# Kernel optimization log

Measured on AMD Instinct MI355X. Metric: run time of the kernel, lower is better.

Reference implementation:

```python
import jax, jax.numpy as jnp
from jax import lax
import numpy as np

N, F_IN, D_MODEL = 8192, 128, 256
D_INNER, D_STATE, D_CONV, DT_RANK = 512, 16, 4, 16  # expand=2, d_state=16, d_conv=4, dt_rank=ceil(256/16)
BN_EPS = 1e-5


def setup_inputs() -> dict:
    key = jax.random.key(0)
    ks = jax.random.split(key, 12)
    rn = lambda k, s, sc: jax.random.normal(k, s, jnp.float32) * sc
    x = rn(ks[0], (N, F_IN), 1.0)
    # normalized dense adjacency (row sums ~1)
    adj = jax.random.uniform(ks[1], (N, N), jnp.float32) * (2.0 / N)
    w_gcn = rn(ks[2], (F_IN, D_MODEL), 1.0 / np.sqrt(F_IN))
    b_gcn = rn(ks[3], (D_MODEL,), 0.02)
    bn_gamma = jnp.ones((D_MODEL,), jnp.float32)
    bn_beta = jnp.zeros((D_MODEL,), jnp.float32)
    w_in = rn(ks[4], (2 * D_INNER, D_MODEL), 1.0 / np.sqrt(D_MODEL))
    conv_w = rn(ks[5], (D_INNER, D_CONV), 1.0 / np.sqrt(D_CONV))
    conv_b = rn(ks[6], (D_INNER,), 0.02)
    w_xproj = rn(ks[7], (DT_RANK + 2 * D_STATE, D_INNER), 1.0 / np.sqrt(D_INNER))
    w_dt = rn(ks[8], (D_INNER, DT_RANK), 1.0 / np.sqrt(DT_RANK))
    b_dt = rn(ks[9], (D_INNER,), 0.1)
    A_log = jnp.log(jnp.broadcast_to(jnp.arange(1, D_STATE + 1, dtype=jnp.float32), (D_INNER, D_STATE)))
    D_skip = jnp.ones((D_INNER,), jnp.float32)
    w_out = rn(ks[10], (D_MODEL, D_INNER), 1.0 / np.sqrt(D_INNER))
    return dict(x=x, adj=adj, w_gcn=w_gcn, b_gcn=b_gcn, bn_gamma=bn_gamma, bn_beta=bn_beta,
                w_in=w_in, conv_w=conv_w, conv_b=conv_b, w_xproj=w_xproj, w_dt=w_dt,
                b_dt=b_dt, A_log=A_log, D_skip=D_skip, w_out=w_out)


def _forward(x, adj, w_gcn, b_gcn, bn_gamma, bn_beta, w_in, conv_w, conv_b,
             w_xproj, w_dt, b_dt, A_log, D_skip, w_out):
    # --- GCN layer: adj @ (x @ W) + b ---
    h = adj @ (x @ w_gcn) + b_gcn            # (N, D_MODEL)
    h = jax.nn.relu(h)
    # dropout: eval mode -> identity
    # --- BatchNorm1d (batch statistics, biased var, as torch training norm) ---
    mean = jnp.mean(h, axis=0)
    var = jnp.var(h, axis=0)
    h = (h - mean) * lax.rsqrt(var + BN_EPS) * bn_gamma + bn_beta  # (N, D_MODEL)

    # --- Mamba block, batch=1, seq_len=N ---
    xz = h @ w_in.T                          # (N, 2*D_INNER)
    xm, z = jnp.split(xz, 2, axis=-1)        # (N, D_INNER) each

    # causal depthwise conv1d (kernel D_CONV) + SiLU
    xp = jnp.pad(xm, ((D_CONV - 1, 0), (0, 0)))
    xc = conv_b + sum(xp[i:i + N] * conv_w[:, i] for i in range(D_CONV))  # (N, D_INNER)
    xc = jax.nn.silu(xc)

    # input-dependent SSM parameters
    x_dbl = xc @ w_xproj.T                   # (N, DT_RANK + 2*D_STATE)
    dt_r = x_dbl[:, :DT_RANK]
    B = x_dbl[:, DT_RANK:DT_RANK + D_STATE]  # (N, D_STATE)
    C = x_dbl[:, DT_RANK + D_STATE:]         # (N, D_STATE)
    dt = jax.nn.softplus(dt_r @ w_dt.T + b_dt)  # (N, D_INNER)

    A = -jnp.exp(A_log)                      # (D_INNER, D_STATE)
    deltaA = jnp.exp(dt[:, :, None] * A[None])                 # (N, D_INNER, D_STATE)
    deltaBu = dt[:, :, None] * B[:, None, :] * xc[:, :, None]  # (N, D_INNER, D_STATE)

    def step(hs, inp):
        dA, dBu, c = inp
        hs = dA * hs + dBu                   # (D_INNER, D_STATE)
        return hs, hs @ c                    # emit (D_INNER,)

    h0 = jnp.zeros((D_INNER, D_STATE), xc.dtype)
    _, ys = lax.scan(step, h0, (deltaA, deltaBu, C))  # ys: (N, D_INNER)

    y = ys + D_skip * xc
    y = y * jax.nn.silu(z)
    out_m = y @ w_out.T                      # (N, D_MODEL)
    return out_m + h                         # residual


def reference(x, adj, w_gcn, b_gcn, bn_gamma, bn_beta, w_in, conv_w, conv_b,
              w_xproj, w_dt, b_dt, A_log, D_skip, w_out):
    return _forward(x, adj, w_gcn, b_gcn, bn_gamma, bn_beta, w_in, conv_w, conv_b,
                    w_xproj, w_dt, b_dt, A_log, D_skip, w_out)
```

## Files before the change

kernel.cpp:

```cpp
#include <hip/hip_runtime.h>
#include <stdint.h>

#define NN   8192
#define FIN  128
#define DM   256
#define DI   512
#define DST  16
#define NC   256
#define CL   32

typedef short bf16x8 __attribute__((ext_vector_type(8)));
typedef float f32x4 __attribute__((ext_vector_type(4)));
union FragU { unsigned u[4]; uint4 u4; bf16x8 v; };

__device__ __forceinline__ unsigned short f2bf(float x){
  unsigned u = __float_as_uint(x);
  return (unsigned short)((u + 0x7FFFu + ((u >> 16) & 1u)) >> 16);
}
__device__ __forceinline__ unsigned pack2(float a, float b){
  return (unsigned)f2bf(a) | ((unsigned)f2bf(b) << 16);
}
__device__ __forceinline__ unsigned pack2rn(float a, float b){
  unsigned ua = __float_as_uint(a) + 0x8000u;
  unsigned ub = __float_as_uint(b) + 0x8000u;
  return __builtin_amdgcn_perm(ub, ua, 0x07060302u);
}
__device__ __forceinline__ uint4 packA8(float4 a, float4 b){
  uint4 w;
  w.x = pack2rn(a.x, a.y); w.y = pack2rn(a.z, a.w);
  w.z = pack2rn(b.x, b.y); w.w = pack2rn(b.z, b.w);
  return w;
}
__device__ __forceinline__ float bf2f(unsigned short u){
  return __uint_as_float(((unsigned)u) << 16);
}
__device__ __forceinline__ float sigmoidf_(float x){ return 1.f / (1.f + __expf(-x)); }
__device__ __forceinline__ f32x4 zero4(){ f32x4 z; z[0]=0.f; z[1]=0.f; z[2]=0.f; z[3]=0.f; return z; }

#define ASYNC16(g, l) __builtin_amdgcn_global_load_lds( \
    (const __attribute__((address_space(1))) void*)(g), \
    (__attribute__((address_space(3))) void*)(l), 16, 0, 0)
#define WAITLGKM0 asm volatile("s_waitcnt lgkmcnt(0)" ::: "memory")
#define BARRIER  asm volatile("s_barrier" ::: "memory")

constexpr size_t OFF_XWT   = 0;
constexpr size_t OFF_HB    = OFF_XWT   + (size_t)DM*NN*2;
constexpr size_t OFF_HBNB  = OFF_HB    + (size_t)NN*DM*2;
constexpr size_t OFF_WINB  = OFF_HBNB  + (size_t)NN*DM*2;
constexpr size_t OFF_WXPB  = OFF_WINB  + (size_t)1024*256*2;
constexpr size_t OFF_WOUTB = OFF_WXPB  + (size_t)48*512*2;
constexpr size_t OFF_XMB   = OFF_WOUTB + (size_t)256*512*2;
constexpr size_t OFF_ZB    = OFF_XMB   + (size_t)NN*DI*2;
constexpr size_t OFF_XCB   = OFF_ZB    + (size_t)NN*DI*2;
constexpr size_t OFF_XDBL  = OFF_XCB   + (size_t)NN*DI*2;
constexpr size_t OFF_DT    = OFF_XDBL  + (size_t)NN*48*4;
constexpr size_t OFF_PF    = OFF_DT    + (size_t)NN*DI*4;
constexpr size_t OFF_CY    = OFF_PF    + (size_t)NC*DI*DST*8;
constexpr size_t OFF_YB    = OFF_CY    + (size_t)NC*DI*DST*4;
constexpr size_t OFF_BNS   = OFF_YB    + (size_t)NN*DI*2;
constexpr size_t OFF_BNS2  = OFF_BNS   + 256*4;
constexpr size_t WS_NEED   = OFF_BNS2  + 256*4;
constexpr size_t OFF_HP    = OFF_PF;

__global__ __launch_bounds__(256) void prep_kernel(
    const float* __restrict__ w_in, const float* __restrict__ w_xp, const float* __restrict__ w_out,
    unsigned short* __restrict__ o_in, unsigned short* __restrict__ o_xp, unsigned short* __restrict__ o_out)
{
  int i = blockIdx.x * 256 + threadIdx.x;
  if (i < 1024*256) o_in[i]  = f2bf(w_in[i]);
  if (i < 48*512)   o_xp[i]  = f2bf(w_xp[i]);
  if (i < 256*512)  o_out[i] = f2bf(w_out[i]);
}

__global__ __launch_bounds__(256) void gemm1_kernel(
    const float* __restrict__ x, const float* __restrict__ w, unsigned short* __restrict__ xwT)
{
  __shared__ float xs[16*128];
  const int t = threadIdx.x;
  const int m0 = blockIdx.x * 16;
  {
    int r = t >> 4, c0 = (t & 15) * 8;
    const float* src = x + (size_t)(m0 + r)*FIN + c0;
    *(float4*)&xs[r*128 + c0]     = *(const float4*)src;
    *(float4*)&xs[r*128 + c0 + 4] = *(const float4*)(src + 4);
  }
  __syncthreads();
  const int n = t;
  float acc[16];
  #pragma unroll
  for (int m = 0; m < 16; ++m) acc[m] = 0.f;
  for (int k = 0; k < 128; k += 4){
    float w0 = w[(size_t)k*DM + n];
    float w1 = w[(size_t)(k+1)*DM + n];
    float w2 = w[(size_t)(k+2)*DM + n];
    float w3 = w[(size_t)(k+3)*DM + n];
    #pragma unroll
    for (int m = 0; m < 16; ++m){
      float4 xv = *(const float4*)&xs[m*128 + k];
      acc[m] = fmaf(xv.x, w0, acc[m]);
      acc[m] = fmaf(xv.y, w1, acc[m]);
      acc[m] = fmaf(xv.z, w2, acc[m]);
      acc[m] = fmaf(xv.w, w3, acc[m]);
    }
  }
  unsigned outp[8];
  #pragma unroll
  for (int m = 0; m < 8; ++m) outp[m] = pack2(acc[2*m], acc[2*m+1]);
  unsigned short* dst = xwT + (size_t)n*NN + m0;
  ((uint4*)dst)[0] = *(uint4*)&outp[0];
  ((uint4*)dst)[1] = *(uint4*)&outp[4];
}

__global__ __launch_bounds__(512, 1) void gemm2_kernel(
    const float* __restrict__ adj, const unsigned short* __restrict__ xwT,
    float* __restrict__ hp)
{
  extern __shared__ char lds[];
  const int t = threadIdx.x;
  const int wave = t >> 6, lane = t & 63, r = lane & 15, q = lane >> 4;
  const int wm = wave & 1, wn = wave >> 1;
  const int mt = (int)blockIdx.x >> 1, ks = (int)blockIdx.x & 1;
  const int m0 = mt * 64;
  const int kb = ks * 4096;

  const int arow = t >> 3, aseg = t & 7;
  const float* asrc = adj + (size_t)(m0 + arow)*NN + kb + aseg*8;
  const int awOff = (arow*32 + ((aseg + arow) & 7)*4) * 4;
  const unsigned short* bsrc[4];
  int bwOff[4];
  #pragma unroll
  for (int j = 0; j < 4; ++j){
    int si = t + 512*j;
    int bn = si >> 3, bc = si & 7;
    bsrc[j]  = xwT + (size_t)bn*NN + kb + bc*8;
    bwOff[j] = 8192 + (bn*32 + ((bc + bn) & 7)*4) * 4;
  }

  f32x4 acc[2][4];
  #pragma unroll
  for (int mi = 0; mi < 2; ++mi)
    #pragma unroll
    for (int ni = 0; ni < 4; ++ni) acc[mi][ni] = zero4();

  int aro[2][2], bro[2][4];
  #pragma unroll
  for (int ks2 = 0; ks2 < 2; ++ks2){
    int g = ks2*4 + q;
    #pragma unroll
    for (int mi = 0; mi < 2; ++mi){
      int m = wm*32 + mi*16 + r;
      aro[ks2][mi] = (m*32 + ((g + m) & 7)*4) * 4;
    }
    #pragma unroll
    for (int ni = 0; ni < 4; ++ni){
      int n = wn*64 + ni*16 + r;
      bro[ks2][ni] = 8192 + (n*32 + ((g + n) & 7)*4) * 4;
    }
  }

  float4 arA[2], arB[2];
  uint4  brr[2][4];

  arA[0] = *(const float4*)(asrc);
  arB[0] = *(const float4*)(asrc + 4);
  #pragma unroll
  for (int j = 0; j < 4; ++j) brr[0][j] = *(const uint4*)(bsrc[j]);
  arA[1] = *(const float4*)(asrc + 64);
  arB[1] = *(const float4*)(asrc + 68);
  #pragma unroll
  for (int j = 0; j < 4; ++j) brr[1][j] = *(const uint4*)(bsrc[j] + 64);
  *(uint4*)(lds + awOff) = packA8(arA[0], arB[0]);
  #pragma unroll
  for (int j = 0; j < 4; ++j) *(uint4*)(lds + bwOff[j]) = brr[0][j];
  WAITLGKM0; BARRIER;

  #pragma unroll 2
  for (int k = 0; k < 64; ++k){
    char* Lb = lds + (k & 1)*40960;
    FragU fa[2][2], fb[2][4];
    #pragma unroll
    for (int ks2 = 0; ks2 < 2; ++ks2){
      #pragma unroll
      for (int mi = 0; mi < 2; ++mi) fa[ks2][mi].u4 = *(const uint4*)(Lb + aro[ks2][mi]);
      #pragma unroll
      for (int ni = 0; ni < 4; ++ni) fb[ks2][ni].u4 = *(const uint4*)(Lb + bro[ks2][ni]);
    }
    if (k + 2 < 64){
      int off = (k + 2) * 64;
      arA[k & 1] = *(const float4*)(asrc + off);
      arB[k & 1] = *(const float4*)(asrc + off + 4);
      #pragma unroll
      for (int j = 0; j < 4; ++j) brr[k & 1][j] = *(const uint4*)(bsrc[j] + off);
    }
    if (k + 1 < 64){
      char* Lw = lds + ((k + 1) & 1)*40960;
      const int b = (k + 1) & 1;
      *(uint4*)(Lw + awOff) = packA8(arA[b], arB[b]);
      #pragma unroll
      for (int j = 0; j < 4; ++j) *(uint4*)(Lw + bwOff[j]) = brr[b][j];
    }
    #pragma unroll
    for (int ks2 = 0; ks2 < 2; ++ks2)
      #pragma unroll
      for (int mi = 0; mi < 2; ++mi)
        #pragma unroll
        for (int ni = 0; ni < 4; ++ni)
          acc[mi][ni] = __builtin_amdgcn_mfma_f32_16x16x32_bf16(fa[ks2][mi].v, fb[ks2][ni].v, acc[mi][ni], 0, 0, 0);
    WAITLGKM0; BARRIER;
  }

  float* hpo = hp + (size_t)ks * ((size_t)NN * DM);
  #pragma unroll
  for (int mi = 0; mi < 2; ++mi)
    #pragma unroll
    for (int ni = 0; ni < 4; ++ni){
      const int n = wn*64 + ni*16 + r;
      #pragma unroll
      for (int jr = 0; jr < 4; ++jr){
        const int m = m0 + wm*32 + mi*16 + q*4 + jr;
        hpo[(size_t)m*DM + n] = acc[mi][ni][jr];
      }
    }
}

__global__ __launch_bounds__(256) void hred_kernel(
    const float* __restrict__ hp, const float* __restrict__ b_gcn,
    unsigned short* __restrict__ hb, float* __restrict__ bns, float* __restrict__ bns2)
{
  const size_t NND = (size_t)NN * DM;
  const int c = threadIdx.x;
  const int m0 = blockIdx.x * 32;
  const float bias = b_gcn[c];
  float s1 = 0.f, s2 = 0.f;
  #pragma unroll 8
  for (int rr = 0; rr < 32; ++rr){
    size_t idx = (size_t)(m0 + rr)*DM + c;
    float v = hp[idx] + hp[NND + idx] + bias;
    v = fmaxf(v, 0.f);
    hb[idx] = f2bf(v);
    s1 += v; s2 += v*v;
  }
  atomicAdd(bns + c, s1);
  atomicAdd(bns2 + c, s2);
}

__global__ __launch_bounds__(256) void bnapply_kernel(
    const unsigned short* __restrict__ hb, const float* __restrict__ s1, const float* __restrict__ s2,
    const float* __restrict__ gamma, const float* __restrict__ beta,
    unsigned short* __restrict__ hbnb)
{
  int base = (blockIdx.x*256 + threadIdx.x) * 2;
  int c0 = base & (DM - 1);
  ushort2 hv = *(const ushort2*)(hb + base);
  float mA = s1[c0] * (1.f/NN),   mB = s1[c0+1] * (1.f/NN);
  float vA = s2[c0] * (1.f/NN) - mA*mA, vB = s2[c0+1] * (1.f/NN) - mB*mB;
  float iA = rsqrtf(vA + 1e-5f), iB = rsqrtf(vB + 1e-5f);
  float a = (bf2f(hv.x) - mA)*iA*gamma[c0]   + beta[c0];
  float b = (bf2f(hv.y) - mB)*iB*gamma[c0+1] + beta[c0+1];
  ushort2 o; o.x = f2bf(a); o.y = f2bf(b);
  *(ushort2*)(hbnb + base) = o;
}

__global__ __launch_bounds__(256) void gemm3_kernel(
    const unsigned short* __restrict__ Ab, const unsigned short* __restrict__ Wb,
    unsigned short* __restrict__ xmb, unsigned short* __restrict__ zb)
{
  __shared__ uint4 alds[2048];
  const int t = threadIdx.x;
  const int wave = t >> 6, lane = t & 63, r = lane & 15, q = lane >> 4;
  const int mb = ((int)blockIdx.x & 127) * 64;
  const int nb = ((int)blockIdx.x >> 7) * 128;
  const int wm = wave & 1, wn = wave >> 1;

  #pragma unroll
  for (int j = 0; j < 8; ++j){
    int si = j*256 + t;
    int row = si >> 5, dg = si & 31;
    int sg = dg ^ (row & 31);
    ASYNC16(Ab + (size_t)(mb + row)*DM + sg*8, (char*)alds + si*16);
  }
  __syncthreads();

  f32x4 acc[2][4];
  #pragma unroll
  for (int mi = 0; mi < 2; ++mi)
    #pragma unroll
    for (int ni = 0; ni < 4; ++ni) acc[mi][ni] = zero4();

  const unsigned short* bp[4];
  #pragma unroll
  for (int ni = 0; ni < 4; ++ni)
    bp[ni] = Wb + (size_t)(nb + wn*64 + ni*16 + r)*DM + q*8;
  FragU fb[4];
  #pragma unroll
  for (int ni = 0; ni < 4; ++ni) fb[ni].u4 = *(const uint4*)bp[ni];

  #pragma unroll
  for (int it = 0; it < 8; ++it){
    FragU fbn[4];
    if (it < 7){
      #pragma unroll
      for (int ni = 0; ni < 4; ++ni) fbn[ni].u4 = *(const uint4*)(bp[ni] + (it+1)*32);
    }
    FragU fa[2];
    #pragma unroll
    for (int mi = 0; mi < 2; ++mi){
      int row = wm*32 + mi*16 + r;
      int g = it*4 + q;
      fa[mi].u4 = alds[row*32 + (g ^ (row & 31))];
    }
    #pragma unroll
    for (int mi = 0; mi < 2; ++mi)
      #pragma unroll
      for (int ni = 0; ni < 4; ++ni)
        acc[mi][ni] = __builtin_amdgcn_mfma_f32_16x16x32_bf16(fa[mi].v, fb[ni].v, acc[mi][ni], 0, 0, 0);
    if (it < 7){
      #pragma unroll
      for (int ni = 0; ni < 4; ++ni) fb[ni] = fbn[ni];
    }
  }
  #pragma unroll
  for (int mi = 0; mi < 2; ++mi)
    #pragma unroll
    for (int ni = 0; ni < 4; ++ni){
      int nc = nb + wn*64 + ni*16 + r;
      unsigned short* dst = (nc < 512) ? (xmb + nc) : (zb + (nc - 512));
      #pragma unroll
      for (int jr = 0; jr < 4; ++jr){
        int m = mb + wm*32 + mi*16 + q*4 + jr;
        dst[(size_t)m*DI] = f2bf(acc[mi][ni][jr]);
      }
    }
}

__global__ __launch_bounds__(256) void conv_kernel(
    const unsigned short* __restrict__ xmb, const float* __restrict__ conv_w, const float* __restrict__ conv_b,
    unsigned short* __restrict__ xcb)
{
  const int d0 = threadIdx.x * 2;
  const int n0 = blockIdx.x * 32;
  float4 wa = *(const float4*)(conv_w + (size_t)d0*4);
  float4 wb = *(const float4*)(conv_w + (size_t)d0*4 + 4);
  float2 bias = *(const float2*)(conv_b + d0);
  float x0a=0.f,x1a=0.f,x2a=0.f, x0b=0.f,x1b=0.f,x2b=0.f;
  #pragma unroll
  for (int j = 0; j < 3; ++j){
    int n = n0 - 3 + j;
    float va = 0.f, vb = 0.f;
    if (n >= 0){
      ushort2 u = *(const ushort2*)(xmb + (size_t)n*DI + d0);
      va = bf2f(u.x); vb = bf2f(u.y);
    }
    if (j == 0){ x0a = va; x0b = vb; }
    else if (j == 1){ x1a = va; x1b = vb; }
    else { x2a = va; x2b = vb; }
  }
  for (int j = 0; j < 32; ++j){
    int n = n0 + j;
    ushort2 u = *(const ushort2*)(xmb + (size_t)n*DI + d0);
    float x3a = bf2f(u.x), x3b = bf2f(u.y);
    float sa = bias.x + wa.x*x0a + wa.y*x1a + wa.z*x2a + wa.w*x3a;
    float sb = bias.y + wb.x*x0b + wb.y*x1b + wb.z*x2b + wb.w*x3b;
    float va = sa * sigmoidf_(sa);
    float vb = sb * sigmoidf_(sb);
    ushort2 o; o.x = f2bf(va); o.y = f2bf(vb);
    *(ushort2*)(xcb + (size_t)n*DI + d0) = o;
    x0a=x1a; x1a=x2a; x2a=x3a;
    x0b=x1b; x1b=x2b; x2b=x3b;
  }
}

__global__ __launch_bounds__(256) void gemm4_kernel(
    const unsigned short* __restrict__ Ab, const unsigned short* __restrict__ Wb,
    const float* __restrict__ w_dt, const float* __restrict__ b_dt,
    float* __restrict__ xdbl, float* __restrict__ dt)
{
  __shared__ uint4 alds[2048];
  __shared__ float xr2[32*16];
  const int t = threadIdx.x;
  const int wave = t >> 6, lane = t & 63, r = lane & 15, q = lane >> 4;
  const int m0 = (int)blockIdx.x * 32;
  #pragma unroll
  for (int j = 0; j < 8; ++j){
    int si = j*256 + t;
    int row = si >> 6, dg = si & 63;
    int sg = dg ^ (row & 31);
    ASYNC16(Ab + (size_t)(m0 + row)*DI + sg*8, (char*)alds + si*16);
  }
  __syncthreads();
  f32x4 acc[2][3];
  #pragma unroll
  for (int mi = 0; mi < 2; ++mi)
    #pragma unroll
    for (int ni = 0; ni < 3; ++ni) acc[mi][ni] = zero4();
  const int kq = wave * 128;
  const unsigned short* bp[3];
  #pragma unroll
  for (int ni = 0; ni < 3; ++ni) bp[ni] = Wb + (size_t)(ni*16 + r)*DI + kq + q*8;
  FragU fb[3];
  #pragma unroll
  for (int ni = 0; ni < 3; ++ni) fb[ni].u4 = *(const uint4*)bp[ni];
  #pragma unroll
  for (int it = 0; it < 4; ++it){
    FragU fbn[3];
    if (it < 3){
      #pragma unroll
      for (int ni = 0; ni < 3; ++ni) fbn[ni].u4 = *(const uint4*)(bp[ni] + (it+1)*32);
    }
    FragU fa[2];
    #pragma unroll
    for (int mi = 0; mi < 2; ++mi){
      int row = mi*16 + r;
      int g = (kq >> 3) + it*4 + q;
      fa[mi].u4 = alds[row*64 + (g ^ (row & 31))];
    }
    #pragma unroll
    for (int mi = 0; mi < 2; ++mi)
      #pragma unroll
      for (int ni = 0; ni < 3; ++ni)
        acc[mi][ni] = __builtin_amdgcn_mfma_f32_16x16x32_bf16(fa[mi].v, fb[ni].v, acc[mi][ni], 0, 0, 0);
    if (it < 3){
      #pragma unroll
      for (int ni = 0; ni < 3; ++ni) fb[ni] = fbn[ni];
    }
  }
  __syncthreads();
  float* red = (float*)alds;
  if (wave > 0){
    int base = ((wave - 1)*64 + lane)*24;
    #pragma unroll
    for (int mi = 0; mi < 2; ++mi)
      #pragma unroll
      for (int ni = 0; ni < 3; ++ni)
        #pragma unroll
        for (int jr = 0; jr < 4; ++jr)
          red[base + (mi*3 + ni)*4 + jr] = acc[mi][ni][jr];
  }
  __syncthreads();
  if (wave == 0){
    #pragma unroll
    for (int w = 0; w < 3; ++w){
      int base = (w*64 + lane)*24;
      #pragma unroll
      for (int mi = 0; mi < 2; ++mi)
        #pragma unroll
        for (int ni = 0; ni < 3; ++ni)
          #pragma unroll
          for (int jr = 0; jr < 4; ++jr)
            acc[mi][ni][jr] += red[base + (mi*3 + ni)*4 + jr];
    }
    #pragma unroll
    for (int mi = 0; mi < 2; ++mi)
      #pragma unroll
      for (int ni = 0; ni < 3; ++ni)
        #pragma unroll
        for (int jr = 0; jr < 4; ++jr)
          xdbl[(size_t)(m0 + mi*16 + q*4 + jr)*48 + ni*16 + r] = acc[mi][ni][jr];
    #pragma unroll
    for (int mi = 0; mi < 2; ++mi)
      #pragma unroll
      for (int jr = 0; jr < 4; ++jr)
        xr2[(mi*16 + q*4 + jr)*16 + r] = acc[mi][0][jr];
  }
  __syncthreads();
  const int d0 = t * 2;
  const float4* wp0 = (const float4*)(w_dt + (size_t)d0*16);
  const float4* wp1 = (const float4*)(w_dt + (size_t)(d0+1)*16);
  float4 wA0 = wp0[0], wA1 = wp0[1], wA2 = wp0[2], wA3 = wp0[3];
  float4 wB0 = wp1[0], wB1 = wp1[1], wB2 = wp1[2], wB3 = wp1[3];
  float2 bb = *(const float2*)(b_dt + d0);
  for (int j = 0; j < 32; ++j){
    const float4* xp = (const float4*)(xr2 + j*16);
    float4 a0 = xp[0], a1 = xp[1], a2 = xp[2], a3 = xp[3];
    float sA = bb.x, sB = bb.y;
    sA += wA0.x*a0.x + wA0.y*a0.y + wA0.z*a0.z + wA0.w*a0.w;
    sA += wA1.x*a1.x + wA1.y*a1.y + wA1.z*a1.z + wA1.w*a1.w;
    sA += wA2.x*a2.x + wA2.y*a2.y + wA2.z*a2.z + wA2.w*a2.w;
    sA += wA3.x*a3.x + wA3.y*a3.y + wA3.z*a3.z + wA3.w*a3.w;
    sB += wB0.x*a0.x + wB0.y*a0.y + wB0.z*a0.z + wB0.w*a0.w;
    sB += wB1.x*a1.x + wB1.y*a1.y + wB1.z*a1.z + wB1.w*a1.w;
    sB += wB2.x*a2.x + wB2.y*a2.y + wB2.z*a2.z + wB2.w*a2.w;
    sB += wB3.x*a3.x + wB3.y*a3.y + wB3.z*a3.z + wB3.w*a3.w;
    float oA = (sA > 20.f) ? sA : log1pf(__expf(sA));
    float oB = (sB > 20.f) ? sB : log1pf(__expf(sB));
    *(float2*)(dt + (size_t)(m0 + j)*DI + d0) = make_float2(oA, oB);
  }
}

__global__ __launch_bounds__(256) void scanA_kernel(
    const float* __restrict__ dt, const unsigned short* __restrict__ xcb,
    const float* __restrict__ xdbl, const float* __restrict__ A_log,
    float2* __restrict__ PF)
{
  __shared__ float Bs[CL*DST];
  const int t = threadIdx.x;
  const int c = (int)blockIdx.x >> 1;
  const int d = (((int)blockIdx.x & 1) << 8) + t;
  #pragma unroll
  for (int j = 0; j < 2; ++j){
    int idx = t + 256*j;
    Bs[idx] = xdbl[(size_t)(c*CL + (idx >> 4))*48 + 16 + (idx & 15)];
  }
  __syncthreads();
  float Av[DST], hs[DST];
  {
    const float4* Ap = (const float4*)(A_log + (size_t)d*DST);
    #pragma unroll
    for (int s4 = 0; s4 < 4; ++s4){
      float4 a4 = Ap[s4];
      Av[s4*4+0] = -__expf(a4.x); Av[s4*4+1] = -__expf(a4.y);
      Av[s4*4+2] = -__expf(a4.z); Av[s4*4+3] = -__expf(a4.w);
    }
  }
  #pragma unroll
  for (int s = 0; s < DST; ++s) hs[s] = 0.f;
  float sdt = 0.f;
  const size_t rb = (size_t)c*CL*DI + d;
  float dtv = dt[rb], xcv = bf2f(xcb[rb]);
  for (int tt = 0; tt < CL; ++tt){
    float dtn = 0.f, xcn = 0.f;
    if (tt + 1 < CL){
      dtn = dt[rb + (size_t)(tt+1)*DI];
      xcn = bf2f(xcb[rb + (size_t)(tt+1)*DI]);
    }
    float u = dtv * xcv;
    sdt += dtv;
    float bv[DST];
    *(float4*)&bv[0]  = *(const float4*)&Bs[tt*16];
    *(float4*)&bv[4]  = *(const float4*)&Bs[tt*16 + 4];
    *(float4*)&bv[8]  = *(const float4*)&Bs[tt*16 + 8];
    *(float4*)&bv[12] = *(const float4*)&Bs[tt*16 + 12];
    #pragma unroll
    for (int s = 0; s < DST; ++s)
      hs[s] = __expf(dtv * Av[s]) * hs[s] + u * bv[s];
    dtv = dtn; xcv = xcn;
  }
  float4* out = (float4*)(PF + (size_t)c*(DI*DST) + (size_t)d*DST);
  #pragma unroll
  for (int j = 0; j < 8; ++j){
    float4 v;
    v.x = __expf(Av[2*j] * sdt);   v.y = hs[2*j];
    v.z = __expf(Av[2*j+1] * sdt); v.w = hs[2*j+1];
    out[j] = v;
  }
}

__global__ __launch_bounds__(128) void scanB_kernel(
    const float2* __restrict__ PF, float* __restrict__ Cy)
{
  const int ds = (int)blockIdx.x*128 + (int)threadIdx.x;
  float2 A0[16], A1[16];
  #pragma unroll
  for (int j = 0; j < 16; ++j) A0[j] = PF[(size_t)j*8192 + ds];
  #pragma unroll
  for (int j = 0; j < 16; ++j) A1[j] = PF[(size_t)(16 + j)*8192 + ds];
  float cy = 0.f;
  Cy[ds] = 0.f;
  #pragma unroll
  for (int g = 0; g < 16; ++g){
    #pragma unroll
    for (int j = 0; j < 16; ++j){
      int i = g*16 + j;
      if (i < NC - 1){
        float2 pf = (g & 1) ? A1[j] : A0[j];
        cy = pf.x * cy + pf.y;
        Cy[(size_t)(i + 1)*8192 + ds] = cy;
      }
    }
    int gn = g + 2;
    if (gn < 16){
      #pragma unroll
      for (int j = 0; j < 16; ++j){
        float2 v = PF[(size_t)(gn*16 + j)*8192 + ds];
        if (g & 1) A1[j] = v; else A0[j] = v;
      }
    }
  }
}

__global__ __launch_bounds__(256) void scanC_kernel(
    const float* __restrict__ dt, const unsigned short* __restrict__ xcb,
    const float* __restrict__ xdbl, const float* __restrict__ A_log,
    const float* __restrict__ Cy, const float* __restrict__ Dskip,
    const unsigned short* __restrict__ zb, unsigned short* __restrict__ yb)
{
  __shared__ float Bs[CL*DST];
  __shared__ float Cs[CL*DST];
  const int t = threadIdx.x;
  const int c = (int)blockIdx.x >> 1;
  const int d = (((int)blockIdx.x & 1) << 8) + t;
  #pragma unroll
  for (int j = 0; j < 2; ++j){
    int idx = t + 256*j;
    int tg = c*CL + (idx >> 4);
    Bs[idx] = xdbl[(size_t)tg*48 + 16 + (idx & 15)];
    Cs[idx] = xdbl[(size_t)tg*48 + 32 + (idx & 15)];
  }
  __syncthreads();
  float Av[DST], hs[DST];
  {
    const float4* Ap = (const float4*)(A_log + (size_t)d*DST);
    #pragma unroll
    for (int s4 = 0; s4 < 4; ++s4){
      float4 a4 = Ap[s4];
      Av[s4*4+0] = -__expf(a4.x); Av[s4*4+1] = -__expf(a4.y);
      Av[s4*4+2] = -__expf(a4.z); Av[s4*4+3] = -__expf(a4.w);
    }
  }
  {
    const float4* hp4 = (const float4*)(Cy + (size_t)c*(DI*DST) + (size_t)d*DST);
    #pragma unroll
    for (int s4 = 0; s4 < 4; ++s4){
      float4 h4 = hp4[s4];
      hs[s4*4+0] = h4.x; hs[s4*4+1] = h4.y; hs[s4*4+2] = h4.z; hs[s4*4+3] = h4.w;
    }
  }
  const float Dv = Dskip[d];
  const size_t rb = (size_t)c*CL*DI + d;
  float dtv = dt[rb], xcv = bf2f(xcb[rb]);
  unsigned short zv0 = zb[rb];
  for (int tt = 0; tt < CL; ++tt){
    float dtn = 0.f, xcn = 0.f;
    unsigned short zn = 0;
    if (tt + 1 < CL){
      dtn = dt[rb + (size_t)(tt+1)*DI];
      xcn = bf2f(xcb[rb + (size_t)(tt+1)*DI]);
      zn  = zb[rb + (size_t)(tt+1)*DI];
    }
    float u = dtv * xcv;
    float bv[DST], cv[DST];
    *(float4*)&bv[0]  = *(const float4*)&Bs[tt*16];
    *(float4*)&bv[4]  = *(const float4*)&Bs[tt*16 + 4];
    *(float4*)&bv[8]  = *(const float4*)&Bs[tt*16 + 8];
    *(float4*)&bv[12] = *(const float4*)&Bs[tt*16 + 12];
    *(float4*)&cv[0]  = *(const float4*)&Cs[tt*16];
    *(float4*)&cv[4]  = *(const float4*)&Cs[tt*16 + 4];
    *(float4*)&cv[8]  = *(const float4*)&Cs[tt*16 + 8];
    *(float4*)&cv[12] = *(const float4*)&Cs[tt*16 + 12];
    float y0 = 0.f, y1 = 0.f;
    #pragma unroll
    for (int s = 0; s < DST; s += 2){
      hs[s]   = __expf(dtv * Av[s])   * hs[s]   + u * bv[s];
      hs[s+1] = __expf(dtv * Av[s+1]) * hs[s+1] + u * bv[s+1];
      y0 += hs[s]   * cv[s];
      y1 += hs[s+1] * cv[s+1];
    }
    float z = bf2f(zv0);
    float yf = ((y0 + y1) + Dv * xcv) * (z * sigmoidf_(z));
    yb[rb + (size_t)tt*DI] = f2bf(yf);
    dtv = dtn; xcv = xcn; zv0 = zn;
  }
}

__global__ __launch_bounds__(512) void gemm5_kernel(
    const unsigned short* __restrict__ yb, const unsigned short* __restrict__ Wb,
    const unsigned short* __restrict__ hbnb, float* __restrict__ out)
{
  __shared__ uint4 alds[2048];
  const int t = threadIdx.x;
  const int wave = t >> 6, lane = t & 63, r = lane & 15, q = lane >> 4;
  const int m0 = (int)blockIdx.x * 32;
  #pragma unroll
  for (int j = 0; j < 4; ++j){
    int si = j*512 + t;
    int row = si >> 6, dg = si & 63;
    int sg = dg ^ (row & 31);
    ASYNC16(yb + (size_t)(m0 + row)*DI + sg*8, (char*)alds + si*16);
  }
  __syncthreads();
  f32x4 acc[2][2];
  #pragma unroll
  for (int mi = 0; mi < 2; ++mi)
    #pragma unroll
    for (int ni = 0; ni < 2; ++ni) acc[mi][ni] = zero4();
  const int nw = wave * 32;
  const unsigned short* bp0 = Wb + (size_t)(nw + r)*DI + q*8;
  const unsigned short* bp1 = Wb + (size_t)(nw + 16 + r)*DI + q*8;
  FragU fb0, fb1;
  fb0.u4 = *(const uint4*)bp0;
  fb1.u4 = *(const uint4*)bp1;
  #pragma unroll
  for (int it = 0; it < 16; ++it){
    FragU fn0, fn1;
    if (it < 15){
      fn0.u4 = *(const uint4*)(bp0 + (it+1)*32);
      fn1.u4 = *(const uint4*)(bp1 + (it+1)*32);
    }
    FragU fa[2];
    #pragma unroll
    for (int mi = 0; mi < 2; ++mi){
      int row = mi*16 + r;
      int g = it*4 + q;
      fa[mi].u4 = alds[row*64 + (g ^ (row & 31))];
    }
    acc[0][0] = __builtin_amdgcn_mfma_f32_16x16x32_bf16(fa[0].v, fb0.v, acc[0][0], 0, 0, 0);
    acc[0][1] = __builtin_amdgcn_mfma_f32_16x16x32_bf16(fa[0].v, fb1.v, acc[0][1], 0, 0, 0);
    acc[1][0] = __builtin_amdgcn_mfma_f32_16x16x32_bf16(fa[1].v, fb0.v, acc[1][0], 0, 0, 0);
    acc[1][1] = __builtin_amdgcn_mfma_f32_16x16x32_bf16(fa[1].v, fb1.v, acc[1][1], 0, 0, 0);
    if (it < 15){ fb0 = fn0; fb1 = fn1; }
  }
  #pragma unroll
  for (int mi = 0; mi < 2; ++mi)
    #pragma unroll
    for (int ni = 0; ni < 2; ++ni){
      const int n = nw + ni*16 + r;
      #pragma unroll
      for (int jr = 0; jr < 4; ++jr){
        const int m = m0 + mi*16 + q*4 + jr;
        size_t idx = (size_t)m*DM + n;
        out[idx] = acc[mi][ni][jr] + bf2f(hbnb[idx]);
      }
    }
}

extern "C" void kernel_launch(void* const* d_in, const int* in_sizes, int n_in,
                              void* d_out, int out_size, void* d_ws, size_t ws_size,
                              hipStream_t stream)
{
  const float* x      = (const float*)d_in[0];
  const float* adj    = (const float*)d_in[1];
  const float* w_gcn  = (const float*)d_in[2];
  const float* b_gcn  = (const float*)d_in[3];
  const float* gamma  = (const float*)d_in[4];
  const float* beta   = (const float*)d_in[5];
  const float* w_in   = (const float*)d_in[6];
  const float* conv_w = (const float*)d_in[7];
  const float* conv_b = (const float*)d_in[8];
  const float* w_xp   = (const float*)d_in[9];
  const float* w_dt   = (const float*)d_in[10];
  const float* b_dt   = (const float*)d_in[11];
  const float* A_log  = (const float*)d_in[12];
  const float* D_skip = (const float*)d_in[13];
  const float* w_out  = (const float*)d_in[14];
  float* out = (float*)d_out;
  char* ws = (char*)d_ws;
  if (ws_size < WS_NEED) return;

  unsigned short* xwT   = (unsigned short*)(ws + OFF_XWT);
  float*          hp    = (float*)(ws + OFF_HP);
  unsigned short* hb    = (unsigned short*)(ws + OFF_HB);
  unsigned short* hbnb  = (unsigned short*)(ws + OFF_HBNB);
  unsigned short* winb  = (unsigned short*)(ws + OFF_WINB);
  unsigned short* wxpb  = (unsigned short*)(ws + OFF_WXPB);
  unsigned short* woutb = (unsigned short*)(ws + OFF_WOUTB);
  unsigned short* xmb   = (unsigned short*)(ws + OFF_XMB);
  unsigned short* zb    = (unsigned short*)(ws + OFF_ZB);
  unsigned short* xcb   = (unsigned short*)(ws + OFF_XCB);
  float*          xdbl  = (float*)(ws + OFF_XDBL);
  float*          dtb   = (float*)(ws + OFF_DT);
  float2*         PF    = (float2*)(ws + OFF_PF);
  float*          Cy    = (float*)(ws + OFF_CY);
  unsigned short* yb    = (unsigned short*)(ws + OFF_YB);
  float*          bns   = (float*)(ws + OFF_BNS);
  float*          bns2  = (float*)(ws + OFF_BNS2);

  hipMemsetAsync(bns, 0, 2*256*sizeof(float), stream);

  hipFuncSetAttribute((const void*)gemm2_kernel,
                      hipFuncAttributeMaxDynamicSharedMemorySize, 81920);

  prep_kernel   <<<1024, 256, 0, stream>>>(w_in, w_xp, w_out, winb, wxpb, woutb);
  gemm1_kernel  <<<512,  256, 0, stream>>>(x, w_gcn, xwT);
  gemm2_kernel  <<<256,  512, 81920, stream>>>(adj, xwT, hp);
  hred_kernel   <<<256,  256, 0, stream>>>(hp, b_gcn, hb, bns, bns2);
  bnapply_kernel<<<4096, 256, 0, stream>>>(hb, bns, bns2, gamma, beta, hbnb);
  gemm3_kernel  <<<1024, 256, 0, stream>>>(hbnb, winb, xmb, zb);
  conv_kernel   <<<256,  256, 0, stream>>>(xmb, conv_w, conv_b, xcb);
  gemm4_kernel  <<<256,  256, 0, stream>>>(xcb, wxpb, w_dt, b_dt, xdbl, dtb);
  scanA_kernel  <<<512,  256, 0, stream>>>(dtb, xcb, xdbl, A_log, PF);
  scanB_kernel  <<<64,   128, 0, stream>>>(PF, Cy);
  scanC_kernel  <<<512,  256, 0, stream>>>(dtb, xcb, xdbl, A_log, Cy, D_skip, zb, yb);
  gemm5_kernel  <<<256,  512, 0, stream>>>(yb, woutb, hbnb, out);
}
```

Baseline: 719.3 us.

## Fold BatchNorm into in-proj weights, drop LDS staging in adjacency GEMM

The BatchNorm apply pass is removed: its per-channel scale is folded into a scaled copy of the in-projection weights, its shift becomes a bias added in the gemm3 epilogue, and the residual is rebuilt in gemm5 from the un-normalized activations plus the scale and shift. The adjacency GEMM now loads A and B fragments straight from global memory into registers with no LDS double buffering or barriers. To support that, gemm1 writes x@W in a K-blocked layout. The scanB launch is also reshaped to more, smaller blocks. Bypassing LDS gives up data sharing between waves, so adjacency rows are re-read by the waves that share them and load latency must be hidden by occupancy alone.

```diff
diff --git a/kernel.cpp b/kernel.cpp
--- a/kernel.cpp
+++ b/kernel.cpp
@@ -25,12 +25,6 @@
   unsigned ub = __float_as_uint(b) + 0x8000u;
   return __builtin_amdgcn_perm(ub, ua, 0x07060302u);
 }
-__device__ __forceinline__ uint4 packA8(float4 a, float4 b){
-  uint4 w;
-  w.x = pack2rn(a.x, a.y); w.y = pack2rn(a.z, a.w);
-  w.z = pack2rn(b.x, b.y); w.w = pack2rn(b.z, b.w);
-  return w;
-}
 __device__ __forceinline__ float bf2f(unsigned short u){
   return __uint_as_float(((unsigned)u) << 16);
 }
@@ -40,14 +34,14 @@
 #define ASYNC16(g, l) __builtin_amdgcn_global_load_lds( \
     (const __attribute__((address_space(1))) void*)(g), \
     (__attribute__((address_space(3))) void*)(l), 16, 0, 0)
-#define WAITLGKM0 asm volatile("s_waitcnt lgkmcnt(0)" ::: "memory")
-#define BARRIER  asm volatile("s_barrier" ::: "memory")
 
 constexpr size_t OFF_XWT   = 0;
 constexpr size_t OFF_HB    = OFF_XWT   + (size_t)DM*NN*2;
-constexpr size_t OFF_HBNB  = OFF_HB    + (size_t)NN*DM*2;
-constexpr size_t OFF_WINB  = OFF_HBNB  + (size_t)NN*DM*2;
-constexpr size_t OFF_WXPB  = OFF_WINB  + (size_t)1024*256*2;
+constexpr size_t OFF_WINB  = OFF_HB    + (size_t)NN*DM*2;
+constexpr size_t OFF_WIN2  = OFF_WINB  + (size_t)1024*256*2;
+constexpr size_t OFF_BIN   = OFF_WIN2  + (size_t)1024*256*2;
+constexpr size_t OFF_AB    = OFF_BIN   + 1024*4;
+constexpr size_t OFF_WXPB  = OFF_AB    + 512*4;
 constexpr size_t OFF_WOUTB = OFF_WXPB  + (size_t)48*512*2;
 constexpr size_t OFF_XMB   = OFF_WOUTB + (size_t)256*512*2;
 constexpr size_t OFF_ZB    = OFF_XMB   + (size_t)NN*DI*2;
@@ -73,7 +67,7 @@
 }
 
 __global__ __launch_bounds__(256) void gemm1_kernel(
-    const float* __restrict__ x, const float* __restrict__ w, unsigned short* __restrict__ xwT)
+    const float* __restrict__ x, const float* __restrict__ w, unsigned short* __restrict__ xwT2)
 {
   __shared__ float xs[16*128];
   const int t = threadIdx.x;
@@ -106,16 +100,15 @@
   unsigned outp[8];
   #pragma unroll
   for (int m = 0; m < 8; ++m) outp[m] = pack2(acc[2*m], acc[2*m+1]);
-  unsigned short* dst = xwT + (size_t)n*NN + m0;
-  ((uint4*)dst)[0] = *(uint4*)&outp[0];
-  ((uint4*)dst)[1] = *(uint4*)&outp[4];
+  unsigned short* dst = xwT2 + (size_t)(m0 >> 3)*2048 + n*8;
+  *(uint4*)dst          = *(uint4*)&outp[0];
+  *(uint4*)(dst + 2048) = *(uint4*)&outp[4];
 }
 
 __global__ __launch_bounds__(512, 1) void gemm2_kernel(
-    const float* __restrict__ adj, const unsigned short* __restrict__ xwT,
+    const float* __restrict__ adj, const unsigned short* __restrict__ xwT2,
     float* __restrict__ hp)
 {
-  extern __shared__ char lds[];
   const int t = threadIdx.x;
   const int wave = t >> 6, lane = t & 63, r = lane & 15, q = lane >> 4;
   const int wm = wave & 1, wn = wave >> 1;
@@ -123,18 +116,12 @@
   const int m0 = mt * 64;
   const int kb = ks * 4096;
 
-  const int arow = t >> 3, aseg = t & 7;
-  const float* asrc = adj + (size_t)(m0 + arow)*NN + kb + aseg*8;
-  const int awOff = (arow*32 + ((aseg + arow) & 7)*4) * 4;
-  const unsigned short* bsrc[4];
-  int bwOff[4];
-  #pragma unroll
-  for (int j = 0; j < 4; ++j){
-    int si = t + 512*j;
-    int bn = si >> 3, bc = si & 7;
-    bsrc[j]  = xwT + (size_t)bn*NN + kb + bc*8;
-    bwOff[j] = 8192 + (bn*32 + ((bc + bn) & 7)*4) * 4;
-  }
+  const float* ap0 = adj + (size_t)(m0 + wm*32 + r)*NN + kb + q*8;
+  const float* ap1 = ap0 + (size_t)16*NN;
+  const unsigned short* bp[4];
+  #pragma unroll
+  for (int ni = 0; ni < 4; ++ni)
+    bp[ni] = xwT2 + ((size_t)(kb >> 3) + q)*2048 + (size_t)(wn*64 + ni*16 + r)*8;
 
   f32x4 acc[2][4];
   #pragma unroll
@@ -142,71 +129,26 @@
     #pragma unroll
     for (int ni = 0; ni < 4; ++ni) acc[mi][ni] = zero4();
 
-  int aro[2][2], bro[2][4];
-  #pragma unroll
-  for (int ks2 = 0; ks2 < 2; ++ks2){
-    int g = ks2*4 + q;
-    #pragma unroll
-    for (int mi = 0; mi < 2; ++mi){
-      int m = wm*32 + mi*16 + r;
-      aro[ks2][mi] = (m*32 + ((g + m) & 7)*4) * 4;
-    }
+  #pragma unroll 4
+  for (int it = 0; it < 128; ++it){
+    float4 a00 = *(const float4*)(ap0 + it*32);
+    float4 a01 = *(const float4*)(ap0 + it*32 + 4);
+    float4 a10 = *(const float4*)(ap1 + it*32);
+    float4 a11 = *(const float4*)(ap1 + it*32 + 4);
+    FragU fb[4];
+    #pragma unroll
+    for (int ni = 0; ni < 4; ++ni)
+      fb[ni].u4 = *(const uint4*)(bp[ni] + (size_t)it*8192);
+    FragU fa0, fa1;
+    fa0.u[0] = pack2rn(a00.x, a00.y); fa0.u[1] = pack2rn(a00.z, a00.w);
+    fa0.u[2] = pack2rn(a01.x, a01.y); fa0.u[3] = pack2rn(a01.z, a01.w);
+    fa1.u[0] = pack2rn(a10.x, a10.y); fa1.u[1] = pack2rn(a10.z, a10.w);
+    fa1.u[2] = pack2rn(a11.x, a11.y); fa1.u[3] = pack2rn(a11.z, a11.w);
     #pragma unroll
     for (int ni = 0; ni < 4; ++ni){
-      int n = wn*64 + ni*16 + r;
-      bro[ks2][ni] = 8192 + (n*32 + ((g + n) & 7)*4) * 4;
-    }
-  }
-
-  float4 arA[2], arB[2];
-  uint4  brr[2][4];
-
-  arA[0] = *(const float4*)(asrc);
-  arB[0] = *(const float4*)(asrc + 4);
-  #pragma unroll
-  for (int j = 0; j < 4; ++j) brr[0][j] = *(const uint4*)(bsrc[j]);
-  arA[1] = *(const float4*)(asrc + 64);
-  arB[1] = *(const float4*)(asrc + 68);
-  #pragma unroll
-  for (int j = 0; j < 4; ++j) brr[1][j] = *(const uint4*)(bsrc[j] + 64);
-  *(uint4*)(lds + awOff) = packA8(arA[0], arB[0]);
-  #pragma unroll
-  for (int j = 0; j < 4; ++j) *(uint4*)(lds + bwOff[j]) = brr[0][j];
-  WAITLGKM0; BARRIER;
-
-  #pragma unroll 2
-  for (int k = 0; k < 64; ++k){
-    char* Lb = lds + (k & 1)*40960;
-    FragU fa[2][2], fb[2][4];
-    #pragma unroll
-    for (int ks2 = 0; ks2 < 2; ++ks2){
-      #pragma unroll
-      for (int mi = 0; mi < 2; ++mi) fa[ks2][mi].u4 = *(const uint4*)(Lb + aro[ks2][mi]);
-      #pragma unroll
-      for (int ni = 0; ni < 4; ++ni) fb[ks2][ni].u4 = *(const uint4*)(Lb + bro[ks2][ni]);
-    }
-    if (k + 2 < 64){
-      int off = (k + 2) * 64;
-      arA[k & 1] = *(const float4*)(asrc + off);
-      arB[k & 1] = *(const float4*)(asrc + off + 4);
-      #pragma unroll
-      for (int j = 0; j < 4; ++j) brr[k & 1][j] = *(const uint4*)(bsrc[j] + off);
-    }
-    if (k + 1 < 64){
-      char* Lw = lds + ((k + 1) & 1)*40960;
-      const int b = (k + 1) & 1;
-      *(uint4*)(Lw + awOff) = packA8(arA[b], arB[b]);
-      #pragma unroll
-      for (int j = 0; j < 4; ++j) *(uint4*)(Lw + bwOff[j]) = brr[b][j];
-    }
-    #pragma unroll
-    for (int ks2 = 0; ks2 < 2; ++ks2)
-      #pragma unroll
-      for (int mi = 0; mi < 2; ++mi)
-        #pragma unroll
-        for (int ni = 0; ni < 4; ++ni)
-          acc[mi][ni] = __builtin_amdgcn_mfma_f32_16x16x32_bf16(fa[ks2][mi].v, fb[ks2][ni].v, acc[mi][ni], 0, 0, 0);
-    WAITLGKM0; BARRIER;
+      acc[0][ni] = __builtin_amdgcn_mfma_f32_16x16x32_bf16(fa0.v, fb[ni].v, acc[0][ni], 0, 0, 0);
+      acc[1][ni] = __builtin_amdgcn_mfma_f32_16x16x32_bf16(fa1.v, fb[ni].v, acc[1][ni], 0, 0, 0);
+    }
   }
 
   float* hpo = hp + (size_t)ks * ((size_t)NN * DM);
@@ -244,25 +186,45 @@
   atomicAdd(bns2 + c, s2);
 }
 
-__global__ __launch_bounds__(256) void bnapply_kernel(
-    const unsigned short* __restrict__ hb, const float* __restrict__ s1, const float* __restrict__ s2,
+__global__ __launch_bounds__(256) void wprep2_kernel(
+    const float* __restrict__ bns, const float* __restrict__ bns2,
     const float* __restrict__ gamma, const float* __restrict__ beta,
-    unsigned short* __restrict__ hbnb)
-{
-  int base = (blockIdx.x*256 + threadIdx.x) * 2;
-  int c0 = base & (DM - 1);
-  ushort2 hv = *(const ushort2*)(hb + base);
-  float mA = s1[c0] * (1.f/NN),   mB = s1[c0+1] * (1.f/NN);
-  float vA = s2[c0] * (1.f/NN) - mA*mA, vB = s2[c0+1] * (1.f/NN) - mB*mB;
-  float iA = rsqrtf(vA + 1e-5f), iB = rsqrtf(vB + 1e-5f);
-  float a = (bf2f(hv.x) - mA)*iA*gamma[c0]   + beta[c0];
-  float b = (bf2f(hv.y) - mB)*iB*gamma[c0+1] + beta[c0+1];
-  ushort2 o; o.x = f2bf(a); o.y = f2bf(b);
-  *(ushort2*)(hbnb + base) = o;
+    const unsigned short* __restrict__ winb,
+    unsigned short* __restrict__ win2, float* __restrict__ binb, float* __restrict__ ab)
+{
+  __shared__ float as_[256], bs_[256];
+  const int t = threadIdx.x;
+  const int n0 = blockIdx.x * 32;
+  float mean = bns[t] * (1.f/NN);
+  float var  = bns2[t] * (1.f/NN) - mean*mean;
+  float inv  = rsqrtf(var + 1e-5f);
+  float a = inv * gamma[t];
+  float b = beta[t] - mean * a;
+  as_[t] = a; bs_[t] = b;
+  if (blockIdx.x == 0){ ab[t] = a; ab[256 + t] = b; }
+  __syncthreads();
+  for (int rr = 0; rr < 32; ++rr){
+    size_t idx = (size_t)(n0 + rr)*256 + t;
+    win2[idx] = f2bf(bf2f(winb[idx]) * as_[t]);
+  }
+  const int wv = t >> 6, ln = t & 63;
+  for (int pass = 0; pass < 8; ++pass){
+    int row = n0 + pass*4 + wv;
+    float v = 0.f;
+    #pragma unroll
+    for (int j = 0; j < 4; ++j){
+      int c = ln*4 + j;
+      v += bs_[c] * bf2f(winb[(size_t)row*256 + c]);
+    }
+    v += __shfl_xor(v, 1);  v += __shfl_xor(v, 2);  v += __shfl_xor(v, 4);
+    v += __shfl_xor(v, 8);  v += __shfl_xor(v, 16); v += __shfl_xor(v, 32);
+    if (ln == 0) binb[row] = v;
+  }
 }
 
 __global__ __launch_bounds__(256) void gemm3_kernel(
     const unsigned short* __restrict__ Ab, const unsigned short* __restrict__ Wb,
+    const float* __restrict__ binb,
     unsigned short* __restrict__ xmb, unsigned short* __restrict__ zb)
 {
   __shared__ uint4 alds[2048];
@@ -324,11 +286,12 @@
     #pragma unroll
     for (int ni = 0; ni < 4; ++ni){
       int nc = nb + wn*64 + ni*16 + r;
+      float bias = binb[nc];
       unsigned short* dst = (nc < 512) ? (xmb + nc) : (zb + (nc - 512));
       #pragma unroll
       for (int jr = 0; jr < 4; ++jr){
         int m = mb + wm*32 + mi*16 + q*4 + jr;
-        dst[(size_t)m*DI] = f2bf(acc[mi][ni][jr]);
+        dst[(size_t)m*DI] = f2bf(acc[mi][ni][jr] + bias);
       }
     }
 }
@@ -545,10 +508,10 @@
   }
 }
 
-__global__ __launch_bounds__(128) void scanB_kernel(
+__global__ __launch_bounds__(64) void scanB_kernel(
     const float2* __restrict__ PF, float* __restrict__ Cy)
 {
-  const int ds = (int)blockIdx.x*128 + (int)threadIdx.x;
+  const int ds = (int)blockIdx.x*64 + (int)threadIdx.x;
   float2 A0[16], A1[16];
   #pragma unroll
   for (int j = 0; j < 16; ++j) A0[j] = PF[(size_t)j*8192 + ds];
@@ -654,7 +617,8 @@
 
 __global__ __launch_bounds__(512) void gemm5_kernel(
     const unsigned short* __restrict__ yb, const unsigned short* __restrict__ Wb,
-    const unsigned short* __restrict__ hbnb, float* __restrict__ out)
+    const unsigned short* __restrict__ hb, const float* __restrict__ ab,
+    float* __restrict__ out)
 {
   __shared__ uint4 alds[2048];
   const int t = threadIdx.x;
@@ -704,11 +668,12 @@
     #pragma unroll
     for (int ni = 0; ni < 2; ++ni){
       const int n = nw + ni*16 + r;
+      const float aA = ab[n], bB = ab[256 + n];
       #pragma unroll
       for (int jr = 0; jr < 4; ++jr){
         const int m = m0 + mi*16 + q*4 + jr;
         size_t idx = (size_t)m*DM + n;
-        out[idx] = acc[mi][ni][jr] + bf2f(hbnb[idx]);
+        out[idx] = acc[mi][ni][jr] + bf2f(hb[idx])*aA + bB;
       }
     }
 }
@@ -736,11 +701,13 @@
   char* ws = (char*)d_ws;
   if (ws_size < WS_NEED) return;
 
-  unsigned short* xwT   = (unsigned short*)(ws + OFF_XWT);
+  unsigned short* xwT2  = (unsigned short*)(ws + OFF_XWT);
   float*          hp    = (float*)(ws + OFF_HP);
   unsigned short* hb    = (unsigned short*)(ws + OFF_HB);
-  unsigned short* hbnb  = (unsigned short*)(ws + OFF_HBNB);
   unsigned short* winb  = (unsigned short*)(ws + OFF_WINB);
+  unsigned short* win2  = (unsigned short*)(ws + OFF_WIN2);
+  float*          binb  = (float*)(ws + OFF_BIN);
+  float*          ab    = (float*)(ws + OFF_AB);
   unsigned short* wxpb  = (unsigned short*)(ws + OFF_WXPB);
   unsigned short* woutb = (unsigned short*)(ws + OFF_WOUTB);
   unsigned short* xmb   = (unsigned short*)(ws + OFF_XMB);
@@ -756,19 +723,16 @@
 
   hipMemsetAsync(bns, 0, 2*256*sizeof(float), stream);
 
-  hipFuncSetAttribute((const void*)gemm2_kernel,
-                      hipFuncAttributeMaxDynamicSharedMemorySize, 81920);
-
   prep_kernel   <<<1024, 256, 0, stream>>>(w_in, w_xp, w_out, winb, wxpb, woutb);
-  gemm1_kernel  <<<512,  256, 0, stream>>>(x, w_gcn, xwT);
-  gemm2_kernel  <<<256,  512, 81920, stream>>>(adj, xwT, hp);
+  gemm1_kernel  <<<512,  256, 0, stream>>>(x, w_gcn, xwT2);
+  gemm2_kernel  <<<256,  512, 0, stream>>>(adj, xwT2, hp);
   hred_kernel   <<<256,  256, 0, stream>>>(hp, b_gcn, hb, bns, bns2);
-  bnapply_kernel<<<4096, 256, 0, stream>>>(hb, bns, bns2, gamma, beta, hbnb);
-  gemm3_kernel  <<<1024, 256, 0, stream>>>(hbnb, winb, xmb, zb);
+  wprep2_kernel <<<32,   256, 0, stream>>>(bns, bns2, gamma, beta, winb, win2, binb, ab);
+  gemm3_kernel  <<<1024, 256, 0, stream>>>(hb, win2, binb, xmb, zb);
   conv_kernel   <<<256,  256, 0, stream>>>(xmb, conv_w, conv_b, xcb);
   gemm4_kernel  <<<256,  256, 0, stream>>>(xcb, wxpb, w_dt, b_dt, xdbl, dtb);
   scanA_kernel  <<<512,  256, 0, stream>>>(dtb, xcb, xdbl, A_log, PF);
-  scanB_kernel  <<<64,   128, 0, stream>>>(PF, Cy);
+  scanB_kernel  <<<128,  64,  0, stream>>>(PF, Cy);
   scanC_kernel  <<<512,  256, 0, stream>>>(dtb, xcb, xdbl, A_log, Cy, D_skip, zb, yb);
-  gemm5_kernel  <<<256,  512, 0, stream>>>(yb, woutb, hbnb, out);
-}
+  gemm5_kernel  <<<256,  512, 0, stream>>>(yb, woutb, hb, ab, out);
+}
```

New measurement: 705.9 us. No clear change (-1.9%).
